# Kernel tuning notes

Measured on AMD Instinct MI355X. Metric: run time of the kernel, lower is better.

The kernel has to match this reference:

```python
import jax, jax.numpy as jnp
import numpy as np

NUM_NODES = 100000
HIDDEN = 128
NUM_EDGES = 800000


def setup_inputs() -> dict:
    key = jax.random.key(0)
    ks = jax.random.split(key, 8)
    s = 1.0 / np.sqrt(HIDDEN)

    def lin_w(k):
        return jax.random.uniform(k, (HIDDEN, HIDDEN), minval=-s, maxval=s, dtype=jnp.float32)

    return {
        "node_id": jnp.arange(NUM_NODES, dtype=jnp.int64) if jax.config.jax_enable_x64 else jnp.arange(NUM_NODES, dtype=jnp.int32),
        "edge_index": jax.random.randint(ks[0], (2, NUM_EDGES), 0, NUM_NODES),
        "emb": jax.random.normal(ks[1], (NUM_NODES, HIDDEN), dtype=jnp.float32),
        "W1l": lin_w(ks[2]), "b1l": jnp.zeros((HIDDEN,), jnp.float32), "W1r": lin_w(ks[3]),
        "W2l": lin_w(ks[4]), "b2l": jnp.zeros((HIDDEN,), jnp.float32), "W2r": lin_w(ks[5]),
        "W3l": lin_w(ks[6]), "b3l": jnp.zeros((HIDDEN,), jnp.float32), "W3r": lin_w(ks[7]),
    }


def reference(node_id, edge_index, emb, W1l, b1l, W1r, W2l, b2l, W2r, W3l, b3l, W3r):
    # x: [N, H] node features from embedding lookup
    x = emb[node_id]
    src, dst = edge_index[0], edge_index[1]

    # in-degree per target node (PyG mean aggregation; zero-degree -> 0 output)
    deg = jax.ops.segment_sum(jnp.ones((NUM_EDGES,), x.dtype), dst, num_segments=NUM_NODES)
    inv_deg = 1.0 / jnp.maximum(deg, 1.0)  # [N]

    def sage_conv(h, Wl, bl, Wr):
        # gather source features [E, H], scatter-sum at targets, then mean
        aggr = jax.ops.segment_sum(h[src], dst, num_segments=NUM_NODES) * inv_deg[:, None]
        # out = lin_l(aggr) + lin_r(h); lin_l has bias, lin_r has none (PyG defaults)
        return aggr @ Wl.T + bl + h @ Wr.T

    x = jax.nn.relu(sage_conv(x, W1l, b1l, W1r))
    # dropout p=0.2 with training=False is identity (eval mode)
    x = jax.nn.relu(sage_conv(x, W2l, b2l, W2r))
    return sage_conv(x, W3l, b3l, W3r)
```

## Files before the change

kernel.cpp:

```cpp
#include <hip/hip_runtime.h>

#define H 128

typedef float v4f __attribute__((ext_vector_type(4)));
typedef short v8s __attribute__((ext_vector_type(8)));


__device__ inline unsigned short bf16_rne(float x) {
  unsigned u = __builtin_bit_cast(unsigned, x);
  unsigned r = u + 0x7FFF + ((u >> 16) & 1);
  return (unsigned short)(r >> 16);
}

__device__ inline void split_bf16(float x, unsigned short& hi, unsigned short& lo) {
  unsigned u = __builtin_bit_cast(unsigned, x);
  unsigned r = u + 0x7FFF + ((u >> 16) & 1);
  hi = (unsigned short)(r >> 16);
  float hf = __builtin_bit_cast(float, r & 0xFFFF0000u);
  float d = x - hf;
  unsigned ud = __builtin_bit_cast(unsigned, d);
  unsigned rd = ud + 0x7FFF + ((ud >> 16) & 1);
  lo = (unsigned short)(rd >> 16);
}



__global__ void hist_kernel(const int* __restrict__ dst, int* __restrict__ deg, int E) {
  int e = blockIdx.x * 256 + threadIdx.x;
  if (e < E) atomicAdd(&deg[dst[e]], 1);
}

__global__ __launch_bounds__(1024) void scan1_kernel(const int* __restrict__ deg,
                                                     int* __restrict__ incl,
                                                     int* __restrict__ blk_sum, int N) {
  __shared__ int lds[1024];
  int t = threadIdx.x;
  int i = blockIdx.x * 1024 + t;
  int v = (i < N) ? deg[i] : 0;
  lds[t] = v;
  __syncthreads();
  for (int off = 1; off < 1024; off <<= 1) {
    int x = (t >= off) ? lds[t - off] : 0;
    __syncthreads();
    lds[t] += x;
    __syncthreads();
  }
  if (i < N) incl[i] = lds[t];
  if (t == 1023) blk_sum[blockIdx.x] = lds[1023];
}

__global__ void scan2_kernel(const int* __restrict__ blk_sum, int* __restrict__ blk_off, int B) {
  __shared__ int lds[256];
  int t = threadIdx.x;
  int v = (t < B) ? blk_sum[t] : 0;
  lds[t] = v;
  __syncthreads();
  for (int off = 1; off < 256; off <<= 1) {
    int x = (t >= off) ? lds[t - off] : 0;
    __syncthreads();
    lds[t] += x;
    __syncthreads();
  }
  blk_off[t] = lds[t] - v;
}

__global__ void rowstart_kernel(const int* __restrict__ incl, const int* __restrict__ deg,
                                const int* __restrict__ blk_off, int* __restrict__ row_start,
                                int N) {
  int i = blockIdx.x * 256 + threadIdx.x;
  if (i < N) row_start[i] = blk_off[i >> 10] + incl[i] - deg[i];
}

__global__ void fill_kernel(const int* __restrict__ src, const int* __restrict__ dst,
                            const int* __restrict__ row_start, int* __restrict__ cursor,
                            int* __restrict__ csr_src, int E) {
  int e = blockIdx.x * 256 + threadIdx.x;
  if (e < E) {
    int d = dst[e];
    int p = atomicAdd(&cursor[d], 1);
    csr_src[row_start[d] + p] = src[e];
  }
}


__global__ void gather_kernel(const float* __restrict__ emb, const int* __restrict__ node_id,
                              unsigned short* __restrict__ hb,
                              unsigned short* __restrict__ hfh,
                              unsigned short* __restrict__ hfl, int N) {
  int i = blockIdx.x * 256 + threadIdx.x;
  if (i < N * 32) {
    int n = i >> 5, g = i & 31;
    float4 v = ((const float4*)emb)[(size_t)node_id[n] * 32 + g];
    float vv[4] = {v.x, v.y, v.z, v.w};
    unsigned short hs[4], ls[4];
#pragma unroll
    for (int k = 0; k < 4; ++k) split_bf16(vv[k], hs[k], ls[k]);
    *(uint2*)(hb + (size_t)n * H + g * 4) =
        make_uint2((unsigned)hs[0] | ((unsigned)hs[1] << 16),
                   (unsigned)hs[2] | ((unsigned)hs[3] << 16));
    size_t fi = (size_t)(n >> 4) * 2048 + (g >> 3) * 512 +
                (((g >> 1) & 3) * 16 + (n & 15)) * 8 + (g & 1) * 4;
    *(uint2*)(hfh + fi) = make_uint2((unsigned)hs[0] | ((unsigned)hs[1] << 16),
                                     (unsigned)hs[2] | ((unsigned)hs[3] << 16));
    *(uint2*)(hfl + fi) = make_uint2((unsigned)ls[0] | ((unsigned)ls[1] << 16),
                                     (unsigned)ls[2] | ((unsigned)ls[3] << 16));
  }
}


__global__ void wsplit_kernel(const float* __restrict__ W0, const float* __restrict__ W1,
                              const float* __restrict__ W2, const float* __restrict__ W3,
                              const float* __restrict__ W4, const float* __restrict__ W5,
                              unsigned short* __restrict__ Wf) {
  int idx = blockIdx.x * 256 + threadIdx.x;
  int sp = idx >> 14;
  int e = idx & 16383;
  const float* src = sp == 0 ? W0 : sp == 1 ? W1 : sp == 2 ? W2
                   : sp == 3 ? W3 : sp == 4 ? W4 : W5;
  int c = e >> 11;
  int kb = (e >> 9) & 3;
  int qq = (e >> 7) & 3;
  int mm = (e >> 3) & 15;
  int j = e & 7;
  int col = c * 16 + mm;
  int k = kb * 32 + qq * 8 + j;
  unsigned short hi, lo;
  split_bf16(src[col * H + k], hi, lo);
  size_t base = (size_t)(sp >> 1) * 65536 + (size_t)(sp & 1) * 32768 + e;
  Wf[base] = hi;
  Wf[base + 16384] = lo;
}


__global__ __launch_bounds__(256) void aggregate_kernel(const unsigned short* __restrict__ hb,
                                                        const int* __restrict__ csr_src,
                                                        const int* __restrict__ row_start,
                                                        const int* __restrict__ deg,
                                                        unsigned short* __restrict__ a_hi,
                                                        unsigned short* __restrict__ a_lo, int N) {
  int node = blockIdx.x * 4 + (threadIdx.x >> 6);
  if (node >= N) return;
  int lane = threadIdx.x & 63;
  int qe = lane >> 4;
  int cl = lane & 15;
  const uint4* __restrict__ h16 = (const uint4*)hb;

  int start = row_start[node];
  int d = deg[node];

  float acc[8] = {0.f, 0.f, 0.f, 0.f, 0.f, 0.f, 0.f, 0.f};

  auto accum = [&](uint4 u) {
    unsigned uu[4] = {u.x, u.y, u.z, u.w};
#pragma unroll
    for (int j = 0; j < 4; ++j) {
      acc[2 * j] += __builtin_bit_cast(float, uu[j] << 16);
      acc[2 * j + 1] += __builtin_bit_cast(float, uu[j] & 0xFFFF0000u);
    }
  };

  int e = qe;
  for (; e + 4 < d; e += 8) {
    int s0 = csr_src[start + e];
    int s1 = csr_src[start + e + 4];
    uint4 u0 = h16[(size_t)s0 * 16 + cl];
    uint4 u1 = h16[(size_t)s1 * 16 + cl];
    accum(u0);
    accum(u1);
  }
  for (; e < d; e += 4) {
    int s = csr_src[start + e];
    accum(h16[(size_t)s * 16 + cl]);
  }

#pragma unroll
  for (int j = 0; j < 8; ++j) {
    acc[j] += __shfl_xor(acc[j], 16);
    acc[j] += __shfl_xor(acc[j], 32);
  }

  float inv = 1.0f / fmaxf((float)d, 1.0f);
  if (qe < 2) {
    unsigned short hs[4], ls[4];
    int b = qe * 4;
#pragma unroll
    for (int j = 0; j < 4; ++j) split_bf16(acc[b + j] * inv, hs[j], ls[j]);
    size_t fi = (size_t)(node >> 4) * 2048 + (cl >> 2) * 512 +
                ((cl & 3) * 16 + (node & 15)) * 8 + qe * 4;
    *(uint2*)(a_hi + fi) = make_uint2((unsigned)hs[0] | ((unsigned)hs[1] << 16),
                                      (unsigned)hs[2] | ((unsigned)hs[3] << 16));
    *(uint2*)(a_lo + fi) = make_uint2((unsigned)ls[0] | ((unsigned)ls[1] << 16),
                                      (unsigned)ls[2] | ((unsigned)ls[3] << 16));
  }
}


template <int RELU, int FINAL>
__global__ __launch_bounds__(256) void gemm_fs(
    const unsigned short* __restrict__ agh, const unsigned short* __restrict__ agl,
    const unsigned short* hfh, const unsigned short* hfl,
    const unsigned short* __restrict__ Wfrag, const float* __restrict__ bias,
    unsigned short* hfh_out, unsigned short* hfl_out, unsigned short* hb_out,
    float* __restrict__ outf, int N) {
  __shared__ __align__(16) unsigned short Wsh[32768];

  int tid = threadIdx.x;
  int wave = tid >> 6, lane = tid & 63;
  int m = lane & 15, q = lane >> 4;
  int T0 = blockIdx.x * 8 + wave * 2;

  v4f acc[16];
#pragma unroll
  for (int t = 0; t < 16; ++t) acc[t] = (v4f){0.f, 0.f, 0.f, 0.f};

  for (int side = 0; side < 2; ++side) {
    const v8s* Wg = (const v8s*)(Wfrag + side * 32768);
    const v8s* XH = (const v8s*)(side ? hfh : agh);
    const v8s* XL = (const v8s*)(side ? hfl : agl);

    __syncthreads();
#pragma unroll
    for (int i = 0; i < 16; ++i) ((v8s*)Wsh)[tid + i * 256] = Wg[tid + i * 256];
    __syncthreads();

    const v8s* WF = (const v8s*)Wsh;
#pragma unroll
    for (int kb = 0; kb < 4; ++kb) {
      v8s ah0 = XH[(size_t)T0 * 256 + kb * 64 + lane];
      v8s ah1 = XH[(size_t)(T0 + 1) * 256 + kb * 64 + lane];
      v8s al0 = XL[(size_t)T0 * 256 + kb * 64 + lane];
      v8s al1 = XL[(size_t)(T0 + 1) * 256 + kb * 64 + lane];
#pragma unroll
      for (int c = 0; c < 8; ++c) {
        v8s bh = WF[c * 256 + kb * 64 + lane];
        v8s bl = WF[2048 + c * 256 + kb * 64 + lane];
        acc[c] = __builtin_amdgcn_mfma_f32_16x16x32_bf16(ah0, bh, acc[c], 0, 0, 0);
        acc[c] = __builtin_amdgcn_mfma_f32_16x16x32_bf16(al0, bh, acc[c], 0, 0, 0);
        acc[c] = __builtin_amdgcn_mfma_f32_16x16x32_bf16(ah0, bl, acc[c], 0, 0, 0);
        acc[8 + c] = __builtin_amdgcn_mfma_f32_16x16x32_bf16(ah1, bh, acc[8 + c], 0, 0, 0);
        acc[8 + c] = __builtin_amdgcn_mfma_f32_16x16x32_bf16(al1, bh, acc[8 + c], 0, 0, 0);
        acc[8 + c] = __builtin_amdgcn_mfma_f32_16x16x32_bf16(ah1, bl, acc[8 + c], 0, 0, 0);
      }
    }
  }

  float bv[8];
#pragma unroll
  for (int c = 0; c < 8; ++c) bv[c] = bias[c * 16 + m];
#pragma unroll
  for (int tr = 0; tr < 2; ++tr) {
    int T = T0 + tr;
#pragma unroll
    for (int c = 0; c < 8; ++c) {
      v4f a = acc[tr * 8 + c];
      size_t fb = (size_t)T * 2048 + (c >> 1) * 512 +
                  (((c & 1) * 2 + (m >> 3)) * 16) * 8 + (m & 7);
#pragma unroll
      for (int i = 0; i < 4; ++i) {
        int row = T * 16 + q * 4 + i;
        if (row < N) {
          float v = a[i] + bv[c];
          if (RELU) v = fmaxf(v, 0.f);
          if (FINAL) {
            outf[(size_t)row * H + c * 16 + m] = v;
          } else {
            unsigned short hi, lo;
            split_bf16(v, hi, lo);
            size_t fi = fb + (q * 4 + i) * 8;
            hfh_out[fi] = hi;
            hfl_out[fi] = lo;
            hb_out[(size_t)row * H + c * 16 + m] = hi;
          }
        }
      }
    }
  }
}


extern "C" void kernel_launch(void* const* d_in, const int* in_sizes, int n_in,
                              void* d_out, int out_size, void* d_ws, size_t ws_size,
                              hipStream_t stream) {
  const int* node_id = (const int*)d_in[0];
  const int* edge_index = (const int*)d_in[1];
  const float* emb = (const float*)d_in[2];
  const float* W1l = (const float*)d_in[3];
  const float* b1l = (const float*)d_in[4];
  const float* W1r = (const float*)d_in[5];
  const float* W2l = (const float*)d_in[6];
  const float* b2l = (const float*)d_in[7];
  const float* W2r = (const float*)d_in[8];
  const float* W3l = (const float*)d_in[9];
  const float* b3l = (const float*)d_in[10];
  const float* W3r = (const float*)d_in[11];

  int N = in_sizes[0];
  int E = in_sizes[1] / 2;
  const int* src = edge_index;
  const int* dst = edge_index + E;

  int ggm = (N + 127) / 128;
  size_t Np = (size_t)ggm * 128;

  char* w = (char*)d_ws;
  auto alloc = [&](size_t bytes) {
    void* p = (void*)w;
    w += (bytes + 255) & ~(size_t)255;
    return p;
  };
  int* deg = (int*)alloc((size_t)N * 4);
  int* cursor = (int*)alloc((size_t)N * 4);
  int* row_start = (int*)alloc((size_t)N * 4);
  int* incl = (int*)alloc((size_t)N * 4);
  int* blk_sum = (int*)alloc(1024);
  int* blk_off = (int*)alloc(1024);
  int* csr_src = (int*)alloc((size_t)E * 4);
  unsigned short* hb = (unsigned short*)alloc((size_t)N * H * 2);
  unsigned short* hfh = (unsigned short*)alloc(Np * H * 2);
  unsigned short* hfl = (unsigned short*)alloc(Np * H * 2);
  unsigned short* agh = (unsigned short*)alloc(Np * H * 2);
  unsigned short* agl = (unsigned short*)alloc(Np * H * 2);
  unsigned short* Wf = (unsigned short*)alloc((size_t)3 * 65536 * 2);

  hipMemsetAsync(deg, 0, (size_t)N * 4, stream);
  hipMemsetAsync(cursor, 0, (size_t)N * 4, stream);

  hist_kernel<<<(E + 255) / 256, 256, 0, stream>>>(dst, deg, E);
  int SB = (N + 1023) / 1024;
  scan1_kernel<<<SB, 1024, 0, stream>>>(deg, incl, blk_sum, N);
  scan2_kernel<<<1, 256, 0, stream>>>(blk_sum, blk_off, SB);
  rowstart_kernel<<<(N + 255) / 256, 256, 0, stream>>>(incl, deg, blk_off, row_start, N);
  fill_kernel<<<(E + 255) / 256, 256, 0, stream>>>(src, dst, row_start, cursor, csr_src, E);

  gather_kernel<<<(N * 32 + 255) / 256, 256, 0, stream>>>(emb, node_id, hb, hfh, hfl, N);
  wsplit_kernel<<<384, 256, 0, stream>>>(W1l, W1r, W2l, W2r, W3l, W3r, Wf);

  int gag = (N + 3) / 4;

  aggregate_kernel<<<gag, 256, 0, stream>>>(hb, csr_src, row_start, deg, agh, agl, N);
  gemm_fs<1, 0><<<ggm, 256, 0, stream>>>(agh, agl, hfh, hfl, Wf + 0 * 65536, b1l,
                                         hfh, hfl, hb, nullptr, N);

  aggregate_kernel<<<gag, 256, 0, stream>>>(hb, csr_src, row_start, deg, agh, agl, N);
  gemm_fs<1, 0><<<ggm, 256, 0, stream>>>(agh, agl, hfh, hfl, Wf + 1 * 65536, b2l,
                                         hfh, hfl, hb, nullptr, N);

  aggregate_kernel<<<gag, 256, 0, stream>>>(hb, csr_src, row_start, deg, agh, agl, N);
  gemm_fs<0, 1><<<ggm, 256, 0, stream>>>(agh, agl, hfh, hfl, Wf + 2 * 65536, b3l,
                                         nullptr, nullptr, nullptr, (float*)d_out, N);
}
```

Baseline: 494.6 us.

## Drop fragment hi-buffer, fuse scan2 into rowstart and gather with weight split

Removes the fragment-layout hi copy of node features: the GEMM now reads the hi part straight from the row-major bf16 buffer and only writes hb plus the lo fragment. scan2 is folded into rowstart, which redoes the small block-offset scan in every block. The gather and weight-split kernels are merged into one launch, and the two memsets become one. These cut launches and one full N×H bf16 write per layer, but the row-major hi loads in the GEMM may coalesce less well than the fragment layout did.

```diff
diff --git a/kernel.cpp b/kernel.cpp
--- a/kernel.cpp
+++ b/kernel.cpp
@@ -49,26 +49,27 @@
   if (t == 1023) blk_sum[blockIdx.x] = lds[1023];
 }
 
-__global__ void scan2_kernel(const int* __restrict__ blk_sum, int* __restrict__ blk_off, int B) {
-  __shared__ int lds[256];
+__global__ void rowstart_kernel(const int* __restrict__ incl, const int* __restrict__ deg,
+                                const int* __restrict__ blk_sum, int* __restrict__ row_start,
+                                int N, int SB) {
+  __shared__ int excl[128];
   int t = threadIdx.x;
-  int v = (t < B) ? blk_sum[t] : 0;
-  lds[t] = v;
+  int v = 0;
+  if (t < 128) {
+    v = (t < SB) ? blk_sum[t] : 0;
+    excl[t] = v;
+  }
   __syncthreads();
-  for (int off = 1; off < 256; off <<= 1) {
-    int x = (t >= off) ? lds[t - off] : 0;
-    __syncthreads();
-    lds[t] += x;
-    __syncthreads();
-  }
-  blk_off[t] = lds[t] - v;
-}
-
-__global__ void rowstart_kernel(const int* __restrict__ incl, const int* __restrict__ deg,
-                                const int* __restrict__ blk_off, int* __restrict__ row_start,
-                                int N) {
-  int i = blockIdx.x * 256 + threadIdx.x;
-  if (i < N) row_start[i] = blk_off[i >> 10] + incl[i] - deg[i];
+  for (int off = 1; off < 128; off <<= 1) {
+    int x = (t >= off && t < 128) ? excl[t - off] : 0;
+    __syncthreads();
+    if (t < 128) excl[t] += x;
+    __syncthreads();
+  }
+  if (t < 128) excl[t] -= v;
+  __syncthreads();
+  int i = blockIdx.x * 256 + t;
+  if (i < N) row_start[i] = excl[i >> 10] + incl[i] - deg[i];
 }
 
 __global__ void fill_kernel(const int* __restrict__ src, const int* __restrict__ dst,
@@ -83,52 +84,46 @@
 }
 
 
-__global__ void gather_kernel(const float* __restrict__ emb, const int* __restrict__ node_id,
-                              unsigned short* __restrict__ hb,
-                              unsigned short* __restrict__ hfh,
-                              unsigned short* __restrict__ hfl, int N) {
-  int i = blockIdx.x * 256 + threadIdx.x;
-  if (i < N * 32) {
-    int n = i >> 5, g = i & 31;
-    float4 v = ((const float4*)emb)[(size_t)node_id[n] * 32 + g];
-    float vv[4] = {v.x, v.y, v.z, v.w};
-    unsigned short hs[4], ls[4];
-#pragma unroll
-    for (int k = 0; k < 4; ++k) split_bf16(vv[k], hs[k], ls[k]);
-    *(uint2*)(hb + (size_t)n * H + g * 4) =
-        make_uint2((unsigned)hs[0] | ((unsigned)hs[1] << 16),
-                   (unsigned)hs[2] | ((unsigned)hs[3] << 16));
-    size_t fi = (size_t)(n >> 4) * 2048 + (g >> 3) * 512 +
-                (((g >> 1) & 3) * 16 + (n & 15)) * 8 + (g & 1) * 4;
-    *(uint2*)(hfh + fi) = make_uint2((unsigned)hs[0] | ((unsigned)hs[1] << 16),
-                                     (unsigned)hs[2] | ((unsigned)hs[3] << 16));
-    *(uint2*)(hfl + fi) = make_uint2((unsigned)ls[0] | ((unsigned)ls[1] << 16),
-                                     (unsigned)ls[2] | ((unsigned)ls[3] << 16));
-  }
-}
-
-
-__global__ void wsplit_kernel(const float* __restrict__ W0, const float* __restrict__ W1,
-                              const float* __restrict__ W2, const float* __restrict__ W3,
-                              const float* __restrict__ W4, const float* __restrict__ W5,
-                              unsigned short* __restrict__ Wf) {
-  int idx = blockIdx.x * 256 + threadIdx.x;
-  int sp = idx >> 14;
-  int e = idx & 16383;
-  const float* src = sp == 0 ? W0 : sp == 1 ? W1 : sp == 2 ? W2
-                   : sp == 3 ? W3 : sp == 4 ? W4 : W5;
-  int c = e >> 11;
-  int kb = (e >> 9) & 3;
-  int qq = (e >> 7) & 3;
-  int mm = (e >> 3) & 15;
-  int j = e & 7;
-  int col = c * 16 + mm;
-  int k = kb * 32 + qq * 8 + j;
-  unsigned short hi, lo;
-  split_bf16(src[col * H + k], hi, lo);
-  size_t base = (size_t)(sp >> 1) * 65536 + (size_t)(sp & 1) * 32768 + e;
-  Wf[base] = hi;
-  Wf[base + 16384] = lo;
+__global__ void gatherw_kernel(const float* __restrict__ emb, const int* __restrict__ node_id,
+                               unsigned short* __restrict__ hb, unsigned short* __restrict__ hfl,
+                               const float* __restrict__ W0, const float* __restrict__ W1,
+                               const float* __restrict__ W2, const float* __restrict__ W3,
+                               const float* __restrict__ W4, const float* __restrict__ W5,
+                               unsigned short* __restrict__ Wf, int N, int GB) {
+  if ((int)blockIdx.x < GB) {
+    int i = blockIdx.x * 256 + threadIdx.x;
+    if (i < N * 32) {
+      int n = i >> 5, g = i & 31;
+      float4 v = ((const float4*)emb)[(size_t)node_id[n] * 32 + g];
+      float vv[4] = {v.x, v.y, v.z, v.w};
+      unsigned short hs[4], ls[4];
+#pragma unroll
+      for (int k = 0; k < 4; ++k) split_bf16(vv[k], hs[k], ls[k]);
+      *(uint2*)(hb + (size_t)n * H + g * 4) =
+          make_uint2((unsigned)hs[0] | ((unsigned)hs[1] << 16),
+                     (unsigned)hs[2] | ((unsigned)hs[3] << 16));
+      size_t fi = (size_t)(n >> 4) * 2048 + (g >> 3) * 512 +
+                  (((g >> 1) & 3) * 16 + (n & 15)) * 8 + (g & 1) * 4;
+      *(uint2*)(hfl + fi) = make_uint2((unsigned)ls[0] | ((unsigned)ls[1] << 16),
+                                       (unsigned)ls[2] | ((unsigned)ls[3] << 16));
+    }
+  } else {
+    int idx = ((int)blockIdx.x - GB) * 256 + threadIdx.x;
+    int sp = idx >> 14;
+    int e = idx & 16383;
+    const float* src = sp == 0 ? W0 : sp == 1 ? W1 : sp == 2 ? W2
+                     : sp == 3 ? W3 : sp == 4 ? W4 : W5;
+    int c = e >> 11;
+    int kb = (e >> 9) & 3;
+    int qq = (e >> 7) & 3;
+    int mm = (e >> 3) & 15;
+    int j = e & 7;
+    unsigned short hi, lo;
+    split_bf16(src[(c * 16 + mm) * H + kb * 32 + qq * 8 + j], hi, lo);
+    size_t base = (size_t)(sp >> 1) * 65536 + (size_t)(sp & 1) * 32768 + e;
+    Wf[base] = hi;
+    Wf[base + 16384] = lo;
+  }
 }
 
 
@@ -198,10 +193,9 @@
 template <int RELU, int FINAL>
 __global__ __launch_bounds__(256) void gemm_fs(
     const unsigned short* __restrict__ agh, const unsigned short* __restrict__ agl,
-    const unsigned short* hfh, const unsigned short* hfl,
+    const unsigned short* hb, const unsigned short* hfl,
     const unsigned short* __restrict__ Wfrag, const float* __restrict__ bias,
-    unsigned short* hfh_out, unsigned short* hfl_out, unsigned short* hb_out,
-    float* __restrict__ outf, int N) {
+    unsigned short* hb_out, unsigned short* hfl_out, float* __restrict__ outf, int N) {
   __shared__ __align__(16) unsigned short Wsh[32768];
 
   int tid = threadIdx.x;
@@ -215,8 +209,6 @@
 
   for (int side = 0; side < 2; ++side) {
     const v8s* Wg = (const v8s*)(Wfrag + side * 32768);
-    const v8s* XH = (const v8s*)(side ? hfh : agh);
-    const v8s* XL = (const v8s*)(side ? hfl : agl);
 
     __syncthreads();
 #pragma unroll
@@ -226,10 +218,21 @@
     const v8s* WF = (const v8s*)Wsh;
 #pragma unroll
     for (int kb = 0; kb < 4; ++kb) {
-      v8s ah0 = XH[(size_t)T0 * 256 + kb * 64 + lane];
-      v8s ah1 = XH[(size_t)(T0 + 1) * 256 + kb * 64 + lane];
-      v8s al0 = XL[(size_t)T0 * 256 + kb * 64 + lane];
-      v8s al1 = XL[(size_t)(T0 + 1) * 256 + kb * 64 + lane];
+      v8s ah0, ah1, al0, al1;
+      if (side == 0) {
+        const v8s* XH = (const v8s*)agh;
+        const v8s* XL = (const v8s*)agl;
+        ah0 = XH[(size_t)T0 * 256 + kb * 64 + lane];
+        ah1 = XH[(size_t)(T0 + 1) * 256 + kb * 64 + lane];
+        al0 = XL[(size_t)T0 * 256 + kb * 64 + lane];
+        al1 = XL[(size_t)(T0 + 1) * 256 + kb * 64 + lane];
+      } else {
+        ah0 = *(const v8s*)(hb + ((size_t)T0 * 16 + m) * H + kb * 32 + q * 8);
+        ah1 = *(const v8s*)(hb + ((size_t)(T0 + 1) * 16 + m) * H + kb * 32 + q * 8);
+        const v8s* XL = (const v8s*)hfl;
+        al0 = XL[(size_t)T0 * 256 + kb * 64 + lane];
+        al1 = XL[(size_t)(T0 + 1) * 256 + kb * 64 + lane];
+      }
 #pragma unroll
       for (int c = 0; c < 8; ++c) {
         v8s bh = WF[c * 256 + kb * 64 + lane];
@@ -266,10 +269,8 @@
           } else {
             unsigned short hi, lo;
             split_bf16(v, hi, lo);
-            size_t fi = fb + (q * 4 + i) * 8;
-            hfh_out[fi] = hi;
-            hfl_out[fi] = lo;
             hb_out[(size_t)row * H + c * 16 + m] = hi;
+            hfl_out[fb + (q * 4 + i) * 8] = lo;
           }
         }
       }
@@ -308,44 +309,41 @@
     w += (bytes + 255) & ~(size_t)255;
     return p;
   };
-  int* deg = (int*)alloc((size_t)N * 4);
-  int* cursor = (int*)alloc((size_t)N * 4);
+  int* deg = (int*)alloc((size_t)2 * N * 4);
+  int* cursor = deg + N;
   int* row_start = (int*)alloc((size_t)N * 4);
   int* incl = (int*)alloc((size_t)N * 4);
   int* blk_sum = (int*)alloc(1024);
-  int* blk_off = (int*)alloc(1024);
   int* csr_src = (int*)alloc((size_t)E * 4);
-  unsigned short* hb = (unsigned short*)alloc((size_t)N * H * 2);
-  unsigned short* hfh = (unsigned short*)alloc(Np * H * 2);
+  unsigned short* hb = (unsigned short*)alloc(Np * H * 2);
   unsigned short* hfl = (unsigned short*)alloc(Np * H * 2);
   unsigned short* agh = (unsigned short*)alloc(Np * H * 2);
   unsigned short* agl = (unsigned short*)alloc(Np * H * 2);
   unsigned short* Wf = (unsigned short*)alloc((size_t)3 * 65536 * 2);
 
-  hipMemsetAsync(deg, 0, (size_t)N * 4, stream);
-  hipMemsetAsync(cursor, 0, (size_t)N * 4, stream);
+  hipMemsetAsync(deg, 0, (size_t)2 * N * 4, stream);
 
   hist_kernel<<<(E + 255) / 256, 256, 0, stream>>>(dst, deg, E);
   int SB = (N + 1023) / 1024;
   scan1_kernel<<<SB, 1024, 0, stream>>>(deg, incl, blk_sum, N);
-  scan2_kernel<<<1, 256, 0, stream>>>(blk_sum, blk_off, SB);
-  rowstart_kernel<<<(N + 255) / 256, 256, 0, stream>>>(incl, deg, blk_off, row_start, N);
+  rowstart_kernel<<<(N + 255) / 256, 256, 0, stream>>>(incl, deg, blk_sum, row_start, N, SB);
   fill_kernel<<<(E + 255) / 256, 256, 0, stream>>>(src, dst, row_start, cursor, csr_src, E);
 
-  gather_kernel<<<(N * 32 + 255) / 256, 256, 0, stream>>>(emb, node_id, hb, hfh, hfl, N);
-  wsplit_kernel<<<384, 256, 0, stream>>>(W1l, W1r, W2l, W2r, W3l, W3r, Wf);
+  int GB = (N * 32 + 255) / 256;
+  gatherw_kernel<<<GB + 384, 256, 0, stream>>>(emb, node_id, hb, hfl,
+                                               W1l, W1r, W2l, W2r, W3l, W3r, Wf, N, GB);
 
   int gag = (N + 3) / 4;
 
   aggregate_kernel<<<gag, 256, 0, stream>>>(hb, csr_src, row_start, deg, agh, agl, N);
-  gemm_fs<1, 0><<<ggm, 256, 0, stream>>>(agh, agl, hfh, hfl, Wf + 0 * 65536, b1l,
-                                         hfh, hfl, hb, nullptr, N);
+  gemm_fs<1, 0><<<ggm, 256, 0, stream>>>(agh, agl, hb, hfl, Wf + 0 * 65536, b1l,
+                                         hb, hfl, nullptr, N);
 
   aggregate_kernel<<<gag, 256, 0, stream>>>(hb, csr_src, row_start, deg, agh, agl, N);
-  gemm_fs<1, 0><<<ggm, 256, 0, stream>>>(agh, agl, hfh, hfl, Wf + 1 * 65536, b2l,
-                                         hfh, hfl, hb, nullptr, N);
+  gemm_fs<1, 0><<<ggm, 256, 0, stream>>>(agh, agl, hb, hfl, Wf + 1 * 65536, b2l,
+                                         hb, hfl, nullptr, N);
 
   aggregate_kernel<<<gag, 256, 0, stream>>>(hb, csr_src, row_start, deg, agh, agl, N);
-  gemm_fs<0, 1><<<ggm, 256, 0, stream>>>(agh, agl, hfh, hfl, Wf + 2 * 65536, b3l,
-                                         nullptr, nullptr, nullptr, (float*)d_out, N);
-}
+  gemm_fs<0, 1><<<ggm, 256, 0, stream>>>(agh, agl, hb, hfl, Wf + 2 * 65536, b3l,
+                                         nullptr, nullptr, (float*)d_out, N);
+}
```

New measurement: 465.9 us. 5.8% less time.

## Fuse CSR construction into one cooperative kernel and merge gather with weight split

Applied to the files above, without the earlier changes.

The separate histogram, two-level scan, row-start and fill kernels plus two memsets are replaced by a single cooperative-groups kernel that uses grid-wide syncs between phases. Cursor is initialised to the row start so the fill writes directly to its final slot. The embedding gather and the weight bf16 split are merged into one launch with a block-index split. This is meant to cut launch count and inter-kernel gaps, but the grid syncs and a single-block scan of chunk sums add serialization, and the fixed 1024-block cooperative grid assumes that many blocks can be co-resident.

```diff
diff --git a/kernel.cpp b/kernel.cpp
--- a/kernel.cpp
+++ b/kernel.cpp
@@ -1,4 +1,7 @@
 #include <hip/hip_runtime.h>
+#include <hip/hip_cooperative_groups.h>
+
+namespace cg = cooperative_groups;
 
 #define H 128
 
@@ -25,110 +28,134 @@
 
 
 
-__global__ void hist_kernel(const int* __restrict__ dst, int* __restrict__ deg, int E) {
-  int e = blockIdx.x * 256 + threadIdx.x;
-  if (e < E) atomicAdd(&deg[dst[e]], 1);
-}
-
-__global__ __launch_bounds__(1024) void scan1_kernel(const int* __restrict__ deg,
-                                                     int* __restrict__ incl,
-                                                     int* __restrict__ blk_sum, int N) {
-  __shared__ int lds[1024];
-  int t = threadIdx.x;
-  int i = blockIdx.x * 1024 + t;
-  int v = (i < N) ? deg[i] : 0;
-  lds[t] = v;
-  __syncthreads();
-  for (int off = 1; off < 1024; off <<= 1) {
-    int x = (t >= off) ? lds[t - off] : 0;
-    __syncthreads();
-    lds[t] += x;
-    __syncthreads();
-  }
-  if (i < N) incl[i] = lds[t];
-  if (t == 1023) blk_sum[blockIdx.x] = lds[1023];
-}
-
-__global__ void scan2_kernel(const int* __restrict__ blk_sum, int* __restrict__ blk_off, int B) {
-  __shared__ int lds[256];
-  int t = threadIdx.x;
-  int v = (t < B) ? blk_sum[t] : 0;
-  lds[t] = v;
-  __syncthreads();
-  for (int off = 1; off < 256; off <<= 1) {
-    int x = (t >= off) ? lds[t - off] : 0;
-    __syncthreads();
-    lds[t] += x;
-    __syncthreads();
-  }
-  blk_off[t] = lds[t] - v;
-}
-
-__global__ void rowstart_kernel(const int* __restrict__ incl, const int* __restrict__ deg,
-                                const int* __restrict__ blk_off, int* __restrict__ row_start,
-                                int N) {
-  int i = blockIdx.x * 256 + threadIdx.x;
-  if (i < N) row_start[i] = blk_off[i >> 10] + incl[i] - deg[i];
-}
-
-__global__ void fill_kernel(const int* __restrict__ src, const int* __restrict__ dst,
-                            const int* __restrict__ row_start, int* __restrict__ cursor,
-                            int* __restrict__ csr_src, int E) {
-  int e = blockIdx.x * 256 + threadIdx.x;
-  if (e < E) {
+__global__ __launch_bounds__(256) void csr_build_kernel(
+    const int* __restrict__ src, const int* __restrict__ dst, int* __restrict__ deg,
+    int* __restrict__ cursor, int* __restrict__ row_start, int* __restrict__ chunk_sum,
+    int* __restrict__ chunk_off, int* __restrict__ csr_src, int N, int E) {
+  cg::grid_group g = cg::this_grid();
+  int tid = threadIdx.x, bid = blockIdx.x, nb = gridDim.x;
+  int gt = bid * 256 + tid, gs = nb * 256;
+  __shared__ int lds[512];
+
+  for (int i = gt; i < N; i += gs) deg[i] = 0;
+  g.sync();
+
+  for (int e = gt; e < E; e += gs) atomicAdd(&deg[dst[e]], 1);
+  g.sync();
+
+  int nch = (N + 255) >> 8;
+  for (int c = bid; c < nch; c += nb) {
+    int i = c * 256 + tid;
+    lds[tid] = (i < N) ? deg[i] : 0;
+    __syncthreads();
+    for (int off = 128; off > 0; off >>= 1) {
+      if (tid < off) lds[tid] += lds[tid + off];
+      __syncthreads();
+    }
+    if (tid == 0) chunk_sum[c] = lds[0];
+    __syncthreads();
+  }
+  g.sync();
+
+  if (bid == 0) {
+    int v0 = (tid < nch) ? chunk_sum[tid] : 0;
+    int v1 = (tid + 256 < nch) ? chunk_sum[tid + 256] : 0;
+    lds[tid] = v0;
+    __syncthreads();
+    for (int off = 1; off < 256; off <<= 1) {
+      int x = (tid >= off) ? lds[tid - off] : 0;
+      __syncthreads();
+      lds[tid] += x;
+      __syncthreads();
+    }
+    int incl0 = lds[tid], total0 = lds[255];
+    __syncthreads();
+    lds[tid] = v1;
+    __syncthreads();
+    for (int off = 1; off < 256; off <<= 1) {
+      int x = (tid >= off) ? lds[tid - off] : 0;
+      __syncthreads();
+      lds[tid] += x;
+      __syncthreads();
+    }
+    int incl1 = lds[tid] + total0;
+    if (tid < nch) chunk_off[tid] = incl0 - v0;
+    if (tid + 256 < nch) chunk_off[tid + 256] = incl1 - v1;
+  }
+  g.sync();
+
+  for (int c = bid; c < nch; c += nb) {
+    int i = c * 256 + tid;
+    int v = (i < N) ? deg[i] : 0;
+    lds[tid] = v;
+    __syncthreads();
+    for (int off = 1; off < 256; off <<= 1) {
+      int x = (tid >= off) ? lds[tid - off] : 0;
+      __syncthreads();
+      lds[tid] += x;
+      __syncthreads();
+    }
+    if (i < N) {
+      int rs = chunk_off[c] + lds[tid] - v;
+      row_start[i] = rs;
+      cursor[i] = rs;
+    }
+    __syncthreads();
+  }
+  g.sync();
+
+  for (int e = gt; e < E; e += gs) {
     int d = dst[e];
     int p = atomicAdd(&cursor[d], 1);
-    csr_src[row_start[d] + p] = src[e];
-  }
-}
-
-
-__global__ void gather_kernel(const float* __restrict__ emb, const int* __restrict__ node_id,
-                              unsigned short* __restrict__ hb,
-                              unsigned short* __restrict__ hfh,
-                              unsigned short* __restrict__ hfl, int N) {
-  int i = blockIdx.x * 256 + threadIdx.x;
-  if (i < N * 32) {
-    int n = i >> 5, g = i & 31;
-    float4 v = ((const float4*)emb)[(size_t)node_id[n] * 32 + g];
-    float vv[4] = {v.x, v.y, v.z, v.w};
-    unsigned short hs[4], ls[4];
-#pragma unroll
-    for (int k = 0; k < 4; ++k) split_bf16(vv[k], hs[k], ls[k]);
-    *(uint2*)(hb + (size_t)n * H + g * 4) =
-        make_uint2((unsigned)hs[0] | ((unsigned)hs[1] << 16),
-                   (unsigned)hs[2] | ((unsigned)hs[3] << 16));
-    size_t fi = (size_t)(n >> 4) * 2048 + (g >> 3) * 512 +
-                (((g >> 1) & 3) * 16 + (n & 15)) * 8 + (g & 1) * 4;
-    *(uint2*)(hfh + fi) = make_uint2((unsigned)hs[0] | ((unsigned)hs[1] << 16),
-                                     (unsigned)hs[2] | ((unsigned)hs[3] << 16));
-    *(uint2*)(hfl + fi) = make_uint2((unsigned)ls[0] | ((unsigned)ls[1] << 16),
-                                     (unsigned)ls[2] | ((unsigned)ls[3] << 16));
-  }
-}
-
-
-__global__ void wsplit_kernel(const float* __restrict__ W0, const float* __restrict__ W1,
-                              const float* __restrict__ W2, const float* __restrict__ W3,
-                              const float* __restrict__ W4, const float* __restrict__ W5,
-                              unsigned short* __restrict__ Wf) {
-  int idx = blockIdx.x * 256 + threadIdx.x;
-  int sp = idx >> 14;
-  int e = idx & 16383;
-  const float* src = sp == 0 ? W0 : sp == 1 ? W1 : sp == 2 ? W2
-                   : sp == 3 ? W3 : sp == 4 ? W4 : W5;
-  int c = e >> 11;
-  int kb = (e >> 9) & 3;
-  int qq = (e >> 7) & 3;
-  int mm = (e >> 3) & 15;
-  int j = e & 7;
-  int col = c * 16 + mm;
-  int k = kb * 32 + qq * 8 + j;
-  unsigned short hi, lo;
-  split_bf16(src[col * H + k], hi, lo);
-  size_t base = (size_t)(sp >> 1) * 65536 + (size_t)(sp & 1) * 32768 + e;
-  Wf[base] = hi;
-  Wf[base + 16384] = lo;
+    csr_src[p] = src[e];
+  }
+}
+
+
+__global__ void gatherw_kernel(const float* __restrict__ emb, const int* __restrict__ node_id,
+                               unsigned short* __restrict__ hb,
+                               unsigned short* __restrict__ hfh,
+                               unsigned short* __restrict__ hfl,
+                               const float* __restrict__ W0, const float* __restrict__ W1,
+                               const float* __restrict__ W2, const float* __restrict__ W3,
+                               const float* __restrict__ W4, const float* __restrict__ W5,
+                               unsigned short* __restrict__ Wf, int N, int GB) {
+  if ((int)blockIdx.x < GB) {
+    int i = blockIdx.x * 256 + threadIdx.x;
+    if (i < N * 32) {
+      int n = i >> 5, g = i & 31;
+      float4 v = ((const float4*)emb)[(size_t)node_id[n] * 32 + g];
+      float vv[4] = {v.x, v.y, v.z, v.w};
+      unsigned short hs[4], ls[4];
+#pragma unroll
+      for (int k = 0; k < 4; ++k) split_bf16(vv[k], hs[k], ls[k]);
+      *(uint2*)(hb + (size_t)n * H + g * 4) =
+          make_uint2((unsigned)hs[0] | ((unsigned)hs[1] << 16),
+                     (unsigned)hs[2] | ((unsigned)hs[3] << 16));
+      size_t fi = (size_t)(n >> 4) * 2048 + (g >> 3) * 512 +
+                  (((g >> 1) & 3) * 16 + (n & 15)) * 8 + (g & 1) * 4;
+      *(uint2*)(hfh + fi) = make_uint2((unsigned)hs[0] | ((unsigned)hs[1] << 16),
+                                       (unsigned)hs[2] | ((unsigned)hs[3] << 16));
+      *(uint2*)(hfl + fi) = make_uint2((unsigned)ls[0] | ((unsigned)ls[1] << 16),
+                                       (unsigned)ls[2] | ((unsigned)ls[3] << 16));
+    }
+  } else {
+    int idx = ((int)blockIdx.x - GB) * 256 + threadIdx.x;
+    int sp = idx >> 14;
+    int e = idx & 16383;
+    const float* srcp = sp == 0 ? W0 : sp == 1 ? W1 : sp == 2 ? W2
+                      : sp == 3 ? W3 : sp == 4 ? W4 : W5;
+    int c = e >> 11;
+    int kb = (e >> 9) & 3;
+    int qq = (e >> 7) & 3;
+    int mm = (e >> 3) & 15;
+    int j = e & 7;
+    unsigned short hi, lo;
+    split_bf16(srcp[(c * 16 + mm) * H + kb * 32 + qq * 8 + j], hi, lo);
+    size_t base = (size_t)(sp >> 1) * 65536 + (size_t)(sp & 1) * 32768 + e;
+    Wf[base] = hi;
+    Wf[base + 16384] = lo;
+  }
 }
 
 
@@ -311,29 +338,27 @@
   int* deg = (int*)alloc((size_t)N * 4);
   int* cursor = (int*)alloc((size_t)N * 4);
   int* row_start = (int*)alloc((size_t)N * 4);
-  int* incl = (int*)alloc((size_t)N * 4);
-  int* blk_sum = (int*)alloc(1024);
-  int* blk_off = (int*)alloc(1024);
+  int* chunk_sum = (int*)alloc(2048);
+  int* chunk_off = (int*)alloc(2048);
   int* csr_src = (int*)alloc((size_t)E * 4);
-  unsigned short* hb = (unsigned short*)alloc((size_t)N * H * 2);
+  unsigned short* hb = (unsigned short*)alloc(Np * H * 2);
   unsigned short* hfh = (unsigned short*)alloc(Np * H * 2);
   unsigned short* hfl = (unsigned short*)alloc(Np * H * 2);
   unsigned short* agh = (unsigned short*)alloc(Np * H * 2);
   unsigned short* agl = (unsigned short*)alloc(Np * H * 2);
   unsigned short* Wf = (unsigned short*)alloc((size_t)3 * 65536 * 2);
 
-  hipMemsetAsync(deg, 0, (size_t)N * 4, stream);
-  hipMemsetAsync(cursor, 0, (size_t)N * 4, stream);
-
-  hist_kernel<<<(E + 255) / 256, 256, 0, stream>>>(dst, deg, E);
-  int SB = (N + 1023) / 1024;
-  scan1_kernel<<<SB, 1024, 0, stream>>>(deg, incl, blk_sum, N);
-  scan2_kernel<<<1, 256, 0, stream>>>(blk_sum, blk_off, SB);
-  rowstart_kernel<<<(N + 255) / 256, 256, 0, stream>>>(incl, deg, blk_off, row_start, N);
-  fill_kernel<<<(E + 255) / 256, 256, 0, stream>>>(src, dst, row_start, cursor, csr_src, E);
-
-  gather_kernel<<<(N * 32 + 255) / 256, 256, 0, stream>>>(emb, node_id, hb, hfh, hfl, N);
-  wsplit_kernel<<<384, 256, 0, stream>>>(W1l, W1r, W2l, W2r, W3l, W3r, Wf);
+  {
+    void* args[] = {(void*)&src,       (void*)&dst,       (void*)&deg,
+                    (void*)&cursor,    (void*)&row_start, (void*)&chunk_sum,
+                    (void*)&chunk_off, (void*)&csr_src,   (void*)&N, (void*)&E};
+    hipLaunchCooperativeKernel((void*)csr_build_kernel, dim3(1024), dim3(256), args, 0,
+                               stream);
+  }
+
+  int GB = (N * 32 + 255) / 256;
+  gatherw_kernel<<<GB + 384, 256, 0, stream>>>(emb, node_id, hb, hfh, hfl,
+                                               W1l, W1r, W2l, W2r, W3l, W3r, Wf, N, GB);
 
   int gag = (N + 3) / 4;
 
```

After: 1.004 ms. 103% more time.
